# Kernel tuning notes

Measured on AMD Instinct MI355X. Metric: run time of the kernel, lower is better.

Reference implementation:

```python
import jax, jax.numpy as jnp
import numpy as np

B, S, D_IN, D, K, KU, L, M, H = 2, 1024, 64, 512, 16, 3, 2, 2, 2048
N_FFT = 2048  # next power of two >= 2*S - 1 (preconvolve padded_sl)
EPS = 1e-5


def setup_inputs() -> dict:
    key = jax.random.key(0)
    ks = jax.random.split(key, 8)
    # Hankel matrix Z[i,j] = 2 / ((i+j)^3 - (i+j)), i,j in 1..S; top-K eigh
    i = np.arange(1, S + 1, dtype=np.float64)
    s = i[:, None] + i[None, :]
    Z = 2.0 / (s ** 3 - s)
    evals, evecs = np.linalg.eigh(Z)
    sigma = jnp.asarray(evals[-K:], jnp.float32)          # (K,)
    phi = jnp.asarray(evecs[:, -K:], jnp.float32)         # (S, K)
    std = D ** -0.5
    return dict(
        inputs=jax.random.normal(ks[0], (B, S, D_IN), jnp.float32),
        sigma=sigma,
        phi=phi,
        in_proj_w=jax.random.normal(ks[1], (M, D, D_IN), jnp.float32) * (D_IN ** -0.5),
        rn_w=jnp.ones((M, L, D), jnp.float32),
        M_u=jax.random.uniform(ks[2], (M, L, KU, D, D), jnp.float32, -std, std),
        M_phi_plus=jax.random.normal(ks[3], (M, L, K, D, D), jnp.float32) * std,
        M_phi_minus=jax.random.normal(ks[4], (M, L, K, D, D), jnp.float32) * std,
        fc1_w=jax.random.normal(ks[5], (M, L, 2 * H, D), jnp.float32) * std,
        fc2_w=jax.random.normal(ks[6], (M, L, D, H), jnp.float32) * (H ** -0.5),
        out_proj_w=jax.random.normal(ks[7], (M, D_IN, D), jnp.float32) * std,
    )


def rmsnorm(x, w):
    return x * jax.lax.rsqrt(jnp.mean(x * x, axis=-1, keepdims=True) + EPS) * w


def compute_spectral(x, sigma, phi, mp, mm):
    # x: (B,S,D); phi: (S,K); mp/mm: (K,D,D)
    sgn = jnp.where(jnp.arange(S) % 2 == 0, 1.0, -1.0).astype(x.dtype)
    u2 = jnp.stack([x, x * sgn[None, :, None]], axis=-1)            # (B,S,D,2)
    U = jnp.fft.rfft(u2, n=N_FFT, axis=1)                           # (B,nf,D,2)
    Vf = jnp.fft.rfft(phi, n=N_FFT, axis=0)                         # (nf,K)
    Uc = jnp.fft.irfft(Vf[None, :, :, None, None] * U[:, :, None, :, :], n=N_FFT, axis=1)[:, :S]  # (B,S,K,D,2)
    Up = Uc[..., 0]
    Um = Uc[..., 1] * sgn[None, :, None, None]
    sig4 = sigma ** 0.25
    return (jnp.einsum('bskd,k,kdo->bso', Up, sig4, mp)
            + jnp.einsum('bskd,k,kdo->bso', Um, sig4, mm))


def compute_ar_u(mu, x):
    # y_t = sum_i x_{t-i} @ M_u[i]; mu: (KU,D,D)
    out = jnp.einsum('bsd,do->bso', x, mu[0])
    for i in range(1, KU):
        xi = jnp.pad(x[:, :S - i], ((0, 0), (i, 0), (0, 0)))
        out = out + jnp.einsum('bsd,do->bso', xi, mu[i])
    return out


def gated_mlp(x, w1, w2):
    y = x @ w1.T
    y, gate = jnp.split(y, 2, axis=-1)
    return (y * jax.nn.silu(gate)) @ w2.T


def reference(inputs, sigma, phi, in_proj_w, rn_w, M_u, M_phi_plus, M_phi_minus, fc1_w, fc2_w, out_proj_w):
    preds = jnp.zeros((B, S, D_IN), inputs.dtype)
    for m in range(M):  # ResidualSTU: sum of per-model predictions
        x = inputs @ in_proj_w[m].T
        for l in range(L):
            z = x
            h = rmsnorm(x, rn_w[m, l])
            spec = compute_spectral(h, sigma, phi, M_phi_plus[m, l], M_phi_minus[m, l])
            y_t = spec + compute_ar_u(M_u[m, l], h)  # use_ar_u=True, use_ar_y=False
            x = x + y_t
            x = x + gated_mlp(x, fc1_w[m, l], fc2_w[m, l])
            x = x + z
        preds = preds + x @ out_proj_w[m].T
    return preds
```

## Files before the change

kernel.cpp:

```cpp
#include <hip/hip_runtime.h>
#include <hip/hip_bf16.h>

typedef _Float16 f16;
typedef _Float16 half8 __attribute__((ext_vector_type(8)));
typedef float f32x4 __attribute__((ext_vector_type(4)));

#define S_LEN 1024
#define DMODEL 512
#define NFFT   2048
#define RPB    2048
#define RTOT   4096
#define CPS    1064
#define NROW   2048
#define NPART  4

__device__ __forceinline__ float2 mkf2(float a, float b) { float2 r; r.x = a; r.y = b; return r; }
__device__ __forceinline__ int zp(int i) { return i + (i >> 5); }

__device__ __forceinline__ void gl16(const f16* g, f16* l) {
  __builtin_amdgcn_global_load_lds((const __attribute__((address_space(1))) void*)g,
                                   (__attribute__((address_space(3))) void*)l, 16, 0, 0);
}

template<bool INV>
__device__ __forceinline__ void fft2048(float2* z, const float2* __restrict__ tw, int tid) {
  for (int i = tid; i < 2048; i += 256) {
    int j = (int)(__brev((unsigned)i) >> 21);
    if (i < j) { float2 a = z[zp(i)]; z[zp(i)] = z[zp(j)]; z[zp(j)] = a; }
  }
  __syncthreads();
#pragma unroll
  for (int sl = 1; sl <= 9; sl += 2) {
    const int h = 1 << (sl - 1);
    for (int q = tid; q < 512; q += 256) {
      int j = q & (h - 1);
      int base = (q >> (sl - 1)) << (sl + 1);
      int i0 = base + j;
      float2 a0 = z[zp(i0)], a1 = z[zp(i0 + h)], a2 = z[zp(i0 + 2 * h)], a3 = z[zp(i0 + 3 * h)];
      float2 w1 = tw[j << (11 - sl)];
      float2 w2 = tw[j << (10 - sl)];
      float2 w3 = tw[(j + h) << (10 - sl)];
      if (INV) { w1.y = -w1.y; w2.y = -w2.y; w3.y = -w3.y; }
      float tr, ti;
      tr = a1.x * w1.x - a1.y * w1.y; ti = a1.x * w1.y + a1.y * w1.x;
      float2 b0 = mkf2(a0.x + tr, a0.y + ti), b1 = mkf2(a0.x - tr, a0.y - ti);
      tr = a3.x * w1.x - a3.y * w1.y; ti = a3.x * w1.y + a3.y * w1.x;
      float2 b2 = mkf2(a2.x + tr, a2.y + ti), b3 = mkf2(a2.x - tr, a2.y - ti);
      tr = b2.x * w2.x - b2.y * w2.y; ti = b2.x * w2.y + b2.y * w2.x;
      z[zp(i0)]         = mkf2(b0.x + tr, b0.y + ti);
      z[zp(i0 + 2 * h)] = mkf2(b0.x - tr, b0.y - ti);
      tr = b3.x * w3.x - b3.y * w3.y; ti = b3.x * w3.y + b3.y * w3.x;
      z[zp(i0 + h)]     = mkf2(b1.x + tr, b1.y + ti);
      z[zp(i0 + 3 * h)] = mkf2(b1.x - tr, b1.y - ti);
    }
    __syncthreads();
  }
  for (int j = tid; j < 1024; j += 256) {
    float2 w = tw[j];
    if (INV) w.y = -w.y;
    float2 a = z[zp(j)], b = z[zp(j + 1024)];
    float tr = b.x * w.x - b.y * w.y, ti = b.x * w.y + b.y * w.x;
    z[zp(j)]        = mkf2(a.x + tr, a.y + ti);
    z[zp(j + 1024)] = mkf2(a.x - tr, a.y - ti);
  }
  __syncthreads();
}

__global__ void k_twiddle(float2* tw) {
  int i = blockIdx.x * 256 + threadIdx.x;
  if (i < 1024) {
    float ang = -6.2831853071795864769f * (float)i / 2048.0f;
    tw[i] = mkf2(cosf(ang), sinf(ang));
  }
}

__global__ void k_fft_phi(const float* __restrict__ phi, float2* __restrict__ Vf,
                          const float2* __restrict__ tw) {
  __shared__ float2 z[2112];
  int tid = threadIdx.x;
  int k0 = blockIdx.x * 2;
  for (int t = tid; t < 1024; t += 256)
    z[zp(t)] = *(const float2*)(phi + (size_t)t * 16 + k0);
  for (int t = 1024 + tid; t < 2048; t += 256) z[zp(t)] = mkf2(0.f, 0.f);
  __syncthreads();
  fft2048<false>(z, tw, tid);
  for (int f = tid; f <= 1024; f += 256) {
    float2 zf = z[zp(f)], zc = z[zp((2048 - f) & 2047)];
    Vf[(size_t)k0 * 1025 + f]       = mkf2(0.5f * (zf.x + zc.x), 0.5f * (zf.y - zc.y));
    Vf[(size_t)(k0 + 1) * 1025 + f] = mkf2(0.5f * (zf.y + zc.y), 0.5f * (zc.x - zf.x));
  }
}

__global__ void k_cpcm(const float2* __restrict__ Vf, const float* __restrict__ sigma,
                       float2* __restrict__ cpcm) {
  int idx = blockIdx.x * 256 + threadIdx.x;
  if (idx >= 32 * CPS) return;
  int kb = idx / CPS, f = idx - kb * CPS;
  int k = kb & 15;
  float s = powf(sigma[k], 0.25f) * (1.0f / 2048.0f);
  float2 v = mkf2(0.f, 0.f);
  if (f == 0) {
    float dc = Vf[(size_t)k * 1025].x;
    float ny = Vf[(size_t)k * 1025 + 1024].x;
    v = (kb < 16) ? mkf2(s * dc, s * ny) : mkf2(s * ny, s * dc);
  } else if (f <= 1023) {
    if (kb < 16) {
      v = Vf[(size_t)k * 1025 + f];
    } else {
      float2 t = Vf[(size_t)k * 1025 + (1024 - f)];
      v = mkf2(t.x, -t.y);
    }
    v.x *= s; v.y *= s;
  }
  cpcm[idx] = v;
}

__global__ void k_cast(const float* __restrict__ mp, const float* __restrict__ mm,
                       const float* __restrict__ mu, const float* __restrict__ fc1,
                       const float* __restrict__ fc2,
                       f16* __restrict__ Wsp, f16* __restrict__ Wu,
                       f16* __restrict__ Wf1, f16* __restrict__ Wf2) {
  __shared__ float T[64][65];
  int blk = blockIdx.x, tid = threadIdx.x;
  if (blk < 2048) {
    int mat = blk >> 6, tile = blk & 63;
    int d0 = (tile >> 3) * 64, o0 = (tile & 7) * 64;
    const float* src = (mat < 16) ? (mp + (size_t)mat * 262144)
                                  : (mm + (size_t)(mat - 16) * 262144);
    for (int q = tid; q < 4096; q += 256) {
      int i = q >> 6, j = q & 63;
      T[i][j] = src[(size_t)(d0 + i) * 512 + o0 + j];
    }
    __syncthreads();
    for (int q = tid; q < 4096; q += 256) {
      int i = q >> 6, j = q & 63;
      Wsp[(size_t)(mat * 512 + o0 + i) * 512 + d0 + j] = (f16)T[j][i];
    }
  } else if (blk < 2240) {
    int q0 = blk - 2048;
    int ip = q0 >> 6, tile = q0 & 63;
    int d0 = (tile >> 3) * 64, o0 = (tile & 7) * 64;
    const float* src = mu + (size_t)(2 - ip) * 262144;
    for (int q = tid; q < 4096; q += 256) {
      int i = q >> 6, j = q & 63;
      T[i][j] = src[(size_t)(d0 + i) * 512 + o0 + j];
    }
    __syncthreads();
    for (int q = tid; q < 4096; q += 256) {
      int i = q >> 6, j = q & 63;
      Wu[(size_t)(o0 + i) * 1536 + ip * 512 + d0 + j] = (f16)T[j][i];
    }
  } else if (blk < 3264) {
    int q0 = blk - 2240;
    size_t e = ((size_t)q0 * 256 + tid) * 8;
    int jj = (int)(e >> 9), col = (int)(e & 511);
    int srow = (jj & 1) ? (2048 + (jj >> 1)) : (jj >> 1);
    const float4* s = (const float4*)(fc1 + (size_t)srow * 512 + col);
    float4 a = s[0], b = s[1];
    union { f16 h[8]; uint4 u; } pk;
    pk.h[0] = (f16)a.x; pk.h[1] = (f16)a.y; pk.h[2] = (f16)a.z; pk.h[3] = (f16)a.w;
    pk.h[4] = (f16)b.x; pk.h[5] = (f16)b.y; pk.h[6] = (f16)b.z; pk.h[7] = (f16)b.w;
    *(uint4*)(Wf1 + (size_t)jj * 512 + col) = pk.u;
  } else {
    int q0 = blk - 3264;
    size_t e = ((size_t)q0 * 256 + tid) * 8;
    const float4* s = (const float4*)(fc2 + e);
    float4 a = s[0], b = s[1];
    union { f16 h[8]; uint4 u; } pk;
    pk.h[0] = (f16)a.x; pk.h[1] = (f16)a.y; pk.h[2] = (f16)a.z; pk.h[3] = (f16)a.w;
    pk.h[4] = (f16)b.x; pk.h[5] = (f16)b.y; pk.h[6] = (f16)b.z; pk.h[7] = (f16)b.w;
    *(uint4*)(Wf2 + e) = pk.u;
  }
}

__global__ void k_rmsnorm(const f16* __restrict__ x, const float* __restrict__ w,
                          f16* __restrict__ hb2) {
  int tid = threadIdx.x, l = tid & 63, wv = tid >> 6;
  int r = blockIdx.x * 4 + wv;
  int b = r >> 10, t = r & 1023;
  const f16* xr = x + (size_t)r * 512;
  f16* hr = hb2 + (size_t)(b * 1026 + 2 + t) * 512;
  float v[8]; float ss = 0.f;
#pragma unroll
  for (int j = 0; j < 8; ++j) { v[j] = (float)xr[j * 64 + l]; ss += v[j] * v[j]; }
#pragma unroll
  for (int o = 32; o; o >>= 1) ss += __shfl_xor(ss, o, 64);
  float rn = rsqrtf(ss * (1.f / 512.f) + 1e-5f);
#pragma unroll
  for (int j = 0; j < 8; ++j) {
    float hv = v[j] * rn * w[j * 64 + l];
    hr[j * 64 + l] = (f16)hv;
  }
}

__global__ void k_fft_fwd(const f16* __restrict__ hb2, f16* __restrict__ Xbf,
                          const float2* __restrict__ tw) {
  __shared__ float2 z[2112];
  int tid = threadIdx.x;
  int b = blockIdx.x >> 8;
  int d0 = (blockIdx.x & 255) * 2;
  for (int t = tid; t < 1024; t += 256) {
    union { unsigned v; f16 q[2]; } w;
    w.v = *(const unsigned*)(hb2 + (size_t)(b * 1026 + 2 + t) * 512 + d0);
    z[zp(t)] = mkf2((float)w.q[0], (float)w.q[1]);
  }
  for (int t = 1024 + tid; t < 2048; t += 256) z[zp(t)] = mkf2(0.f, 0.f);
  __syncthreads();
  fft2048<false>(z, tw, tid);
  for (int f = tid; f <= 1024; f += 256) {
    float2 zf = z[zp(f)], zc = z[zp((2048 - f) & 2047)];
    float x0r = 0.5f * (zf.x + zc.x), x0i = 0.5f * (zf.y - zc.y);
    float x1r = 0.5f * (zf.y + zc.y), x1i = 0.5f * (zc.x - zf.x);
    union { f16 h2[2]; unsigned u; } pr, pi;
    pr.h2[0] = (f16)x0r; pr.h2[1] = (f16)x1r;
    pi.h2[0] = (f16)x0i; pi.h2[1] = (f16)x1i;
    if (f == 0) {
      *(unsigned*)(Xbf + (size_t)(b * RPB) * 512 + d0) = pr.u;
    } else if (f == 1024) {
      *(unsigned*)(Xbf + (size_t)(b * RPB + 1) * 512 + d0) = pr.u;
    } else {
      *(unsigned*)(Xbf + (size_t)(b * RPB + 2 * f) * 512 + d0)     = pr.u;
      *(unsigned*)(Xbf + (size_t)(b * RPB + 2 * f + 1) * 512 + d0) = pi.u;
    }
  }
}

__global__ void k_fft_inv(const f16* __restrict__ P, f16* __restrict__ spec,
                          const float2* __restrict__ tw) {
  __shared__ float2 z[2112];
  int tid = threadIdx.x;
  int b = blockIdx.x >> 8;
  int o0 = (blockIdx.x & 255) * 2;
  for (int fp = tid; fp < 512; fp += 256) {
    int f0 = fp * 2;
    size_t base0 = (size_t)o0 * RTOT + (size_t)b * RPB + 2 * f0;
    float s0r[2] = {0.f, 0.f}, s0i[2] = {0.f, 0.f};
    float s1r[2] = {0.f, 0.f}, s1i[2] = {0.f, 0.f};
#pragma unroll
    for (int g = 0; g < NPART; ++g) {
      const f16* Pg = P + (size_t)g * 512 * RTOT;
      union { uint2 u; f16 h[4]; } ua, uc;
      ua.u = *(const uint2*)(Pg + base0);
      uc.u = *(const uint2*)(Pg + base0 + RTOT);
      s0r[0] += (float)ua.h[0]; s0i[0] += (float)ua.h[1];
      s0r[1] += (float)ua.h[2]; s0i[1] += (float)ua.h[3];
      s1r[0] += (float)uc.h[0]; s1i[0] += (float)uc.h[1];
      s1r[1] += (float)uc.h[2]; s1i[1] += (float)uc.h[3];
    }
    if (fp == 0) {
      z[zp(0)]    = mkf2(s0r[0], s1r[0]);
      z[zp(1024)] = mkf2(s0i[0], s1i[0]);
    } else {
      z[zp(f0)]        = mkf2(s0r[0] - s1i[0], s0i[0] + s1r[0]);
      z[zp(2048 - f0)] = mkf2(s0r[0] + s1i[0], s1r[0] - s0i[0]);
    }
    int f1 = f0 + 1;
    z[zp(f1)]        = mkf2(s0r[1] - s1i[1], s0i[1] + s1r[1]);
    z[zp(2048 - f1)] = mkf2(s0r[1] + s1i[1], s1r[1] - s0i[1]);
  }
  __syncthreads();
  fft2048<true>(z, tw, tid);
  for (int t = tid; t < 1024; t += 256) {
    float2 v = z[zp(t)];
    union { f16 h[2]; unsigned u; } pk;
    pk.h[0] = (f16)v.x; pk.h[1] = (f16)v.y;
    *(unsigned*)(spec + (size_t)(b * 1024 + t) * 512 + o0) = pk.u;
  }
}

template<int MODE, int MR, int NR>
__device__ __forceinline__ void stage(const f16* __restrict__ A, const f16* __restrict__ B0,
                                      int r0, int c0, int bz, int tid, int s,
                                      f16* As, f16* Bs) {
  constexpr int LDA = (MODE == 0) ? 512 : (MODE == 1) ? 1536 : (MODE == 2) ? 512 : 2048;
  const int kA = (MODE == 0) ? ((s & 7) * 64) : s * 64;
  const int rowl = tid >> 3;
  const int lc8 = ((tid & 7) ^ (rowl & 7)) * 8;
  f16* lA = As + ((tid >> 6) << 9);
  f16* lB = Bs + ((tid >> 6) << 9);
#pragma unroll
  for (int i = 0; i < MR; ++i) {
    int row = i * 32 + rowl;
    gl16(A + (size_t)(r0 + row) * LDA + kA + lc8, lA + i * 2048);
  }
#pragma unroll
  for (int i = 0; i < NR; ++i) {
    int row = i * 32 + rowl;
    const f16* bs;
    if constexpr (MODE == 0) {
      int kb = bz * 8 + (s >> 3);
      bs = B0 + (size_t)(kb * 512 + c0 + row) * 512 + (s & 7) * 64 + lc8;
    } else if constexpr (MODE == 1) {
      int ip = s >> 3, d0 = (s & 7) * 64;
      int rr = c0 + row;
      int b = rr >> 10, t = rr & 1023;
      bs = B0 + (size_t)(b * 1026 + t + ip) * 512 + d0 + lc8;
    } else {
      constexpr int LDB = (MODE == 2) ? 512 : 2048;
      bs = B0 + (size_t)(c0 + row) * LDB + s * 64 + lc8;
    }
    gl16(bs, lB + i * 2048);
  }
}

template<int MR, int NR>
__device__ __forceinline__ void mma_step(const f16* As, const f16* Bs, int l, int wr, int wc,
                                         f32x4 acc[MR][NR]) {
  const int lr = l & 15, kg = l >> 4, sw = l & 7;
#pragma unroll
  for (int kk = 0; kk < 2; ++kk) {
    half8 af[MR], bf[NR];
    const int pc8 = (((kk * 4 + kg) ^ sw) << 3);
#pragma unroll
    for (int m = 0; m < MR; ++m)
      af[m] = *(const half8*)(As + (wr * (MR * 16) + m * 16 + lr) * 64 + pc8);
#pragma unroll
    for (int n = 0; n < NR; ++n)
      bf[n] = *(const half8*)(Bs + (wc * (NR * 16) + n * 16 + lr) * 64 + pc8);
#pragma unroll
    for (int m = 0; m < MR; ++m)
#pragma unroll
      for (int n = 0; n < NR; ++n)
        acc[m][n] = __builtin_amdgcn_mfma_f32_16x16x32_f16(af[m], bf[n], acc[m][n], 0, 0, 0);
  }
}

template<int MODE, int MR, int NR>
__global__ __launch_bounds__(256, (MODE == 0) ? 2 : ((MODE == 2) ? 3 : 4))
void k_gemm(const f16* __restrict__ A, const f16* __restrict__ B0,
            const float* __restrict__ aux0, const f16* auxA, const f16* auxB,
            f16* __restrict__ outH) {
  __shared__ __align__(16) f16 As[MR * 32 * 64];
  __shared__ __align__(16) f16 Bs[NR * 32 * 64];
  const int tid = threadIdx.x, l = tid & 63, wvi = tid >> 6;
  const int wr = wvi >> 1, wc = wvi & 1;
  int bx, by, bz;
  if constexpr (MODE == 0) {
    int wg = (int)blockIdx.x;
    wg = (wg & 7) * 64 + (wg >> 3);
    bz = wg >> 7; int rem = wg & 127;
    by = rem >> 2; bx = rem & 3;
  } else { bx = blockIdx.x; by = blockIdx.y; bz = 0; }
  const int r0 = by * (MR * 32), c0 = bx * (NR * 32);
  constexpr int KS = (MODE == 0) ? 64 : (MODE == 1) ? 24 : (MODE == 2) ? 8 : 32;

  f32x4 acc[MR][NR];
  f32x4 crun[MR][NR];
  f32x4 zz = {0.f, 0.f, 0.f, 0.f};
#pragma unroll
  for (int m = 0; m < MR; ++m)
#pragma unroll
    for (int n = 0; n < NR; ++n) { acc[m][n] = zz; crun[m][n] = zz; }

  for (int s = 0; s < KS; ++s) {
    __syncthreads();
    stage<MODE, MR, NR>(A, B0, r0, c0, bz, tid, s, As, Bs);
    __syncthreads();
    mma_step<MR, NR>(As, Bs, l, wr, wc, acc);
    if constexpr (MODE == 0) {
      if ((s & 7) == 7) {
        int kb = bz * 8 + (s >> 3);
#pragma unroll
        for (int m = 0; m < MR; ++m) {
          int R = r0 + wr * (MR * 16) + m * 16 + ((l >> 4) << 2);
          int rb = R & (RPB - 1);
          bool dc = (rb == 0);
          float4 cs = *(const float4*)(aux0 + (size_t)kb * (CPS * 2) + (rb >> 1) * 2);
          float t1 = dc ? 0.f : cs.y;
          float t2 = dc ? cs.y : cs.x;
#pragma unroll
          for (int n = 0; n < NR; ++n) {
            f32x4 p = acc[m][n];
            crun[m][n].x += cs.x * p.x - t1 * p.y;
            crun[m][n].y += t2 * p.y + t1 * p.x;
            crun[m][n].z += cs.z * p.z - cs.w * p.w;
            crun[m][n].w += cs.z * p.w + cs.w * p.z;
            acc[m][n] = zz;
          }
        }
      }
    }
  }

  if constexpr (MODE == 0) {
    f16* P = outH + (size_t)bz * (512ull * RTOT);
#pragma unroll
    for (int m = 0; m < MR; ++m) {
      int R0 = r0 + wr * (MR * 16) + m * 16 + ((l >> 4) << 2);
#pragma unroll
      for (int n = 0; n < NR; ++n) {
        int o = c0 + wc * (NR * 16) + n * 16 + (l & 15);
        union { f16 h[4]; uint2 u; } pk;
        pk.h[0] = (f16)crun[m][n].x; pk.h[1] = (f16)crun[m][n].y;
        pk.h[2] = (f16)crun[m][n].z; pk.h[3] = (f16)crun[m][n].w;
        *(uint2*)(P + (size_t)o * RTOT + R0) = pk.u;
      }
    }
  } else if constexpr (MODE == 1) {
#pragma unroll
    for (int m = 0; m < MR; ++m) {
      int o0 = r0 + wr * (MR * 16) + m * 16 + ((l >> 4) << 2);
#pragma unroll
      for (int n = 0; n < NR; ++n) {
        int r = c0 + wc * (NR * 16) + n * 16 + (l & 15);
        union { uint2 u; f16 h[4]; } xv, sv;
        xv.u = *(const uint2*)(auxA + (size_t)r * 512 + o0);
        sv.u = *(const uint2*)(auxB + (size_t)r * 512 + o0);
        f32x4 a = acc[m][n];
        union { f16 h[4]; uint2 u; } pk;
        pk.h[0] = (f16)((float)xv.h[0] + (float)sv.h[0] + a.x);
        pk.h[1] = (f16)((float)xv.h[1] + (float)sv.h[1] + a.y);
        pk.h[2] = (f16)((float)xv.h[2] + (float)sv.h[2] + a.z);
        pk.h[3] = (f16)((float)xv.h[3] + (float)sv.h[3] + a.w);
        *(uint2*)(outH + (size_t)r * 512 + o0) = pk.u;
      }
    }
  } else if constexpr (MODE == 2) {
#pragma unroll
    for (int m = 0; m < MR; ++m) {
      int jj0 = r0 + wr * (MR * 16) + m * 16 + ((l >> 4) << 2);
      int h2 = jj0 >> 1;
#pragma unroll
      for (int n = 0; n < NR; ++n) {
        int r = c0 + wc * (NR * 16) + n * 16 + (l & 15);
        f32x4 a = acc[m][n];
        float v0 = a.x * (a.y / (1.f + __expf(-a.y)));
        float v1 = a.z * (a.w / (1.f + __expf(-a.w)));
        union { f16 h[2]; unsigned u; } pk;
        pk.h[0] = (f16)v0; pk.h[1] = (f16)v1;
        *(unsigned*)(outH + (size_t)r * 2048 + h2) = pk.u;
      }
    }
  } else {
#pragma unroll
    for (int m = 0; m < MR; ++m) {
      int o0 = r0 + wr * (MR * 16) + m * 16 + ((l >> 4) << 2);
#pragma unroll
      for (int n = 0; n < NR; ++n) {
        int r = c0 + wc * (NR * 16) + n * 16 + (l & 15);
        union { uint2 u; f16 h[4]; } xv, x1v;
        xv.u  = *(const uint2*)(auxA + (size_t)r * 512 + o0);
        x1v.u = *(const uint2*)(auxB + (size_t)r * 512 + o0);
        f32x4 a = acc[m][n];
        union { f16 h[4]; uint2 u; } pk;
        pk.h[0] = (f16)((float)xv.h[0] + (float)x1v.h[0] + a.x);
        pk.h[1] = (f16)((float)xv.h[1] + (float)x1v.h[1] + a.y);
        pk.h[2] = (f16)((float)xv.h[2] + (float)x1v.h[2] + a.z);
        pk.h[3] = (f16)((float)xv.h[3] + (float)x1v.h[3] + a.w);
        *(uint2*)(outH + (size_t)r * 512 + o0) = pk.u;
      }
    }
  }
}

__global__ void k_inproj(const float* __restrict__ inp, const float* __restrict__ W,
                         f16* __restrict__ x) {
  __shared__ float row[64];
  int r = blockIdx.x, tid = threadIdx.x;
  if (tid < 64) row[tid] = inp[(size_t)r * 64 + tid];
  __syncthreads();
  for (int o = tid; o < 512; o += 256) {
    const float* wr = W + (size_t)o * 64;
    float acc = 0.f;
#pragma unroll 8
    for (int q = 0; q < 64; ++q) acc += row[q] * wr[q];
    x[(size_t)r * 512 + o] = (f16)acc;
  }
}

__global__ void k_outproj(const f16* __restrict__ x, const float* __restrict__ W,
                          float* out, int add) {
  __shared__ float row[512];
  int r = blockIdx.x, tid = threadIdx.x;
  for (int i = tid; i < 512; i += 256) row[i] = (float)x[(size_t)r * 512 + i];
  __syncthreads();
  int o = tid >> 2, part = tid & 3;
  const float* wr = W + (size_t)o * 512 + part * 128;
  const float* rp = row + part * 128;
  float acc = 0.f;
#pragma unroll 16
  for (int q = 0; q < 128; ++q) acc += rp[q] * wr[q];
  acc += __shfl_xor(acc, 1, 64);
  acc += __shfl_xor(acc, 2, 64);
  if (part == 0) {
    if (add) out[(size_t)r * 64 + o] += acc;
    else     out[(size_t)r * 64 + o] = acc;
  }
}

extern "C" void kernel_launch(void* const* d_in, const int* in_sizes, int n_in,
                              void* d_out, int out_size, void* d_ws, size_t ws_size,
                              hipStream_t stream) {
  const float* inputs    = (const float*)d_in[0];
  const float* sigma     = (const float*)d_in[1];
  const float* phi       = (const float*)d_in[2];
  const float* in_proj_w = (const float*)d_in[3];
  const float* rn_w      = (const float*)d_in[4];
  const float* M_u       = (const float*)d_in[5];
  const float* M_phi_p   = (const float*)d_in[6];
  const float* M_phi_m   = (const float*)d_in[7];
  const float* fc1       = (const float*)d_in[8];
  const float* fc2       = (const float*)d_in[9];
  const float* out_proj_w= (const float*)d_in[10];
  float* out = (float*)d_out;

  char* ws = (char*)d_ws;
  size_t off = 0;
  auto alloc = [&](size_t bytes) -> void* {
    void* p = ws + off;
    off += (bytes + 255) & ~(size_t)255;
    return p;
  };
  float2* tw   = (float2*)alloc(1024 * 8);
  float2* Vf   = (float2*)alloc((size_t)16 * 1025 * 8);
  float2* cpcm = (float2*)alloc((size_t)32 * CPS * 8);
  f16*    x    = (f16*)alloc((size_t)NROW * 512 * 2);
  f16*    hb2  = (f16*)alloc((size_t)2052 * 512 * 2);
  f16*    x1   = (f16*)alloc((size_t)NROW * 512 * 2);
  f16*    spec = (f16*)alloc((size_t)NROW * 512 * 2);
  f16*    Xbf  = (f16*)alloc((size_t)RTOT * 512 * 2);
  f16*    P    = (f16*)alloc((size_t)NPART * 512 * RTOT * 2);
  f16*    g1   = (f16*)alloc((size_t)NROW * 2048 * 2);
  f16*    Wsp  = (f16*)alloc((size_t)16384 * 512 * 2);
  f16*    Wu   = (f16*)alloc((size_t)512 * 1536 * 2);
  f16*    Wf1  = (f16*)alloc((size_t)4096 * 512 * 2);
  f16*    Wf2  = (f16*)alloc((size_t)512 * 2048 * 2);
  if (off > ws_size) return;

  hipMemsetAsync(hb2, 0, 2 * 512 * sizeof(f16), stream);
  hipMemsetAsync(hb2 + (size_t)1026 * 512, 0, 2 * 512 * sizeof(f16), stream);
  k_twiddle<<<4, 256, 0, stream>>>(tw);
  k_fft_phi<<<8, 256, 0, stream>>>(phi, Vf, tw);
  k_cpcm<<<133, 256, 0, stream>>>(Vf, sigma, cpcm);

  for (int m = 0; m < 2; ++m) {
    k_inproj<<<NROW, 256, 0, stream>>>(inputs, in_proj_w + (size_t)m * 512 * 64, x);
    for (int li = 0; li < 2; ++li) {
      int ml = m * 2 + li;
      k_cast<<<3776, 256, 0, stream>>>(
          M_phi_p + (size_t)ml * 16 * 262144, M_phi_m + (size_t)ml * 16 * 262144,
          M_u + (size_t)ml * 3 * 262144, fc1 + (size_t)ml * 4096 * 512,
          fc2 + (size_t)ml * 512 * 2048, Wsp, Wu, Wf1, Wf2);
      k_rmsnorm<<<512, 256, 0, stream>>>(x, rn_w + (size_t)ml * 512, hb2);
      k_fft_fwd<<<512, 256, 0, stream>>>(hb2, Xbf, tw);
      k_gemm<0, 4, 4><<<dim3(512), 256, 0, stream>>>(Xbf, Wsp, (const float*)cpcm,
                                                     nullptr, nullptr, P);
      k_fft_inv<<<512, 256, 0, stream>>>(P, spec, tw);
      k_gemm<1, 2, 2><<<dim3(32, 8), 256, 0, stream>>>(Wu, hb2, nullptr, x, spec, x1);
      k_gemm<2, 4, 4><<<dim3(16, 32), 256, 0, stream>>>(Wf1, x1, nullptr,
                                                        nullptr, nullptr, g1);
      k_gemm<3, 2, 2><<<dim3(32, 8), 256, 0, stream>>>(Wf2, g1, nullptr, x, x1, x);
    }
    k_outproj<<<NROW, 256, 0, stream>>>(x, out_proj_w + (size_t)m * 64 * 512, out, m);
  }
}
```

Before: 853.2 us.

## Use radix-8 FFT stages and fuse forward FFT with weight cast kernel

The 2048-point FFT now runs three radix-8 passes plus a final radix-4 pass instead of five radix-4 passes plus a radix-2 pass, which cuts the number of barriers and shared-memory round trips. The forward FFT is also merged into the weight-cast kernel as extra workgroups, with rmsnorm moved ahead of it. This lets the FFT work overlap with the memory-bound cast and removes one launch. The radix-8 butterflies need more registers per thread, and the merged kernel's shared-memory size is set by the larger of its two branches.

```diff
diff --git a/kernel.cpp b/kernel.cpp
--- a/kernel.cpp
+++ b/kernel.cpp
@@ -16,6 +16,11 @@
 
 __device__ __forceinline__ float2 mkf2(float a, float b) { float2 r; r.x = a; r.y = b; return r; }
 __device__ __forceinline__ int zp(int i) { return i + (i >> 5); }
+__device__ __forceinline__ float2 cmul(float2 w, float2 b) {
+  return mkf2(b.x * w.x - b.y * w.y, b.x * w.y + b.y * w.x);
+}
+__device__ __forceinline__ float2 f2a(float2 a, float2 b) { return mkf2(a.x + b.x, a.y + b.y); }
+__device__ __forceinline__ float2 f2s(float2 a, float2 b) { return mkf2(a.x - b.x, a.y - b.y); }
 
 __device__ __forceinline__ void gl16(const f16* g, f16* l) {
   __builtin_amdgcn_global_load_lds((const __attribute__((address_space(1))) void*)g,
@@ -30,38 +35,53 @@
   }
   __syncthreads();
 #pragma unroll
-  for (int sl = 1; sl <= 9; sl += 2) {
+  for (int r8 = 0; r8 < 3; ++r8) {
+    const int sl = 1 + 3 * r8;
     const int h = 1 << (sl - 1);
-    for (int q = tid; q < 512; q += 256) {
+    {
+      int q = tid;
       int j = q & (h - 1);
-      int base = (q >> (sl - 1)) << (sl + 1);
-      int i0 = base + j;
-      float2 a0 = z[zp(i0)], a1 = z[zp(i0 + h)], a2 = z[zp(i0 + 2 * h)], a3 = z[zp(i0 + 3 * h)];
-      float2 w1 = tw[j << (11 - sl)];
-      float2 w2 = tw[j << (10 - sl)];
-      float2 w3 = tw[(j + h) << (10 - sl)];
-      if (INV) { w1.y = -w1.y; w2.y = -w2.y; w3.y = -w3.y; }
-      float tr, ti;
-      tr = a1.x * w1.x - a1.y * w1.y; ti = a1.x * w1.y + a1.y * w1.x;
-      float2 b0 = mkf2(a0.x + tr, a0.y + ti), b1 = mkf2(a0.x - tr, a0.y - ti);
-      tr = a3.x * w1.x - a3.y * w1.y; ti = a3.x * w1.y + a3.y * w1.x;
-      float2 b2 = mkf2(a2.x + tr, a2.y + ti), b3 = mkf2(a2.x - tr, a2.y - ti);
-      tr = b2.x * w2.x - b2.y * w2.y; ti = b2.x * w2.y + b2.y * w2.x;
-      z[zp(i0)]         = mkf2(b0.x + tr, b0.y + ti);
-      z[zp(i0 + 2 * h)] = mkf2(b0.x - tr, b0.y - ti);
-      tr = b3.x * w3.x - b3.y * w3.y; ti = b3.x * w3.y + b3.y * w3.x;
-      z[zp(i0 + h)]     = mkf2(b1.x + tr, b1.y + ti);
-      z[zp(i0 + 3 * h)] = mkf2(b1.x - tr, b1.y - ti);
+      int i0 = ((q >> (sl - 1)) << (sl + 2)) + j;
+      float2 a0 = z[zp(i0)],         a1 = z[zp(i0 + h)];
+      float2 a2 = z[zp(i0 + 2 * h)], a3 = z[zp(i0 + 3 * h)];
+      float2 a4 = z[zp(i0 + 4 * h)], a5 = z[zp(i0 + 5 * h)];
+      float2 a6 = z[zp(i0 + 6 * h)], a7 = z[zp(i0 + 7 * h)];
+      float2 wA  = tw[j << (11 - sl)];
+      float2 wB0 = tw[j << (10 - sl)];
+      float2 wB1 = tw[(j + h) << (10 - sl)];
+      float2 wC0 = tw[j << (9 - sl)];
+      float2 wC1 = tw[(j + h) << (9 - sl)];
+      float2 wC2 = tw[(j + 2 * h) << (9 - sl)];
+      float2 wC3 = tw[(j + 3 * h) << (9 - sl)];
+      if (INV) {
+        wA.y = -wA.y; wB0.y = -wB0.y; wB1.y = -wB1.y;
+        wC0.y = -wC0.y; wC1.y = -wC1.y; wC2.y = -wC2.y; wC3.y = -wC3.y;
+      }
+      float2 t;
+      t = cmul(wA, a1); float2 b0 = f2a(a0, t), b1 = f2s(a0, t);
+      t = cmul(wA, a3); float2 b2 = f2a(a2, t), b3 = f2s(a2, t);
+      t = cmul(wA, a5); float2 b4 = f2a(a4, t), b5 = f2s(a4, t);
+      t = cmul(wA, a7); float2 b6 = f2a(a6, t), b7 = f2s(a6, t);
+      t = cmul(wB0, b2); float2 c0 = f2a(b0, t), c2 = f2s(b0, t);
+      t = cmul(wB1, b3); float2 c1 = f2a(b1, t), c3 = f2s(b1, t);
+      t = cmul(wB0, b6); float2 c4 = f2a(b4, t), c6 = f2s(b4, t);
+      t = cmul(wB1, b7); float2 c5 = f2a(b5, t), c7 = f2s(b5, t);
+      t = cmul(wC0, c4); z[zp(i0)]         = f2a(c0, t); z[zp(i0 + 4 * h)] = f2s(c0, t);
+      t = cmul(wC1, c5); z[zp(i0 + h)]     = f2a(c1, t); z[zp(i0 + 5 * h)] = f2s(c1, t);
+      t = cmul(wC2, c6); z[zp(i0 + 2 * h)] = f2a(c2, t); z[zp(i0 + 6 * h)] = f2s(c2, t);
+      t = cmul(wC3, c7); z[zp(i0 + 3 * h)] = f2a(c3, t); z[zp(i0 + 7 * h)] = f2s(c3, t);
     }
     __syncthreads();
   }
-  for (int j = tid; j < 1024; j += 256) {
-    float2 w = tw[j];
-    if (INV) w.y = -w.y;
-    float2 a = z[zp(j)], b = z[zp(j + 1024)];
-    float tr = b.x * w.x - b.y * w.y, ti = b.x * w.y + b.y * w.x;
-    z[zp(j)]        = mkf2(a.x + tr, a.y + ti);
-    z[zp(j + 1024)] = mkf2(a.x - tr, a.y - ti);
+  for (int q = tid; q < 512; q += 256) {
+    float2 a0 = z[zp(q)], a1 = z[zp(q + 512)], a2 = z[zp(q + 1024)], a3 = z[zp(q + 1536)];
+    float2 w1 = tw[q << 1], w2 = tw[q], w3 = tw[q + 512];
+    if (INV) { w1.y = -w1.y; w2.y = -w2.y; w3.y = -w3.y; }
+    float2 t;
+    t = cmul(w1, a1); float2 b0 = f2a(a0, t), b1 = f2s(a0, t);
+    t = cmul(w1, a3); float2 b2 = f2a(a2, t), b3 = f2s(a2, t);
+    t = cmul(w2, b2); z[zp(q)]        = f2a(b0, t); z[zp(q + 1024)] = f2s(b0, t);
+    t = cmul(w3, b3); z[zp(q + 512)]  = f2a(b1, t); z[zp(q + 1536)] = f2s(b1, t);
   }
   __syncthreads();
 }
@@ -115,13 +135,48 @@
   cpcm[idx] = v;
 }
 
-__global__ void k_cast(const float* __restrict__ mp, const float* __restrict__ mm,
-                       const float* __restrict__ mu, const float* __restrict__ fc1,
-                       const float* __restrict__ fc2,
-                       f16* __restrict__ Wsp, f16* __restrict__ Wu,
-                       f16* __restrict__ Wf1, f16* __restrict__ Wf2) {
-  __shared__ float T[64][65];
-  int blk = blockIdx.x, tid = threadIdx.x;
+__global__ __launch_bounds__(256)
+void k_fwdcast(const f16* __restrict__ hb2, f16* __restrict__ Xbf,
+               const float2* __restrict__ tw,
+               const float* __restrict__ mp, const float* __restrict__ mm,
+               const float* __restrict__ mu, const float* __restrict__ fc1,
+               const float* __restrict__ fc2,
+               f16* __restrict__ Wsp, f16* __restrict__ Wu,
+               f16* __restrict__ Wf1, f16* __restrict__ Wf2) {
+  __shared__ __align__(16) char smem[16896];
+  int wg = (int)blockIdx.x, tid = threadIdx.x;
+  if (wg < 512) {
+    float2* z = (float2*)smem;
+    int b = wg >> 8;
+    int d0 = (wg & 255) * 2;
+    for (int t = tid; t < 1024; t += 256) {
+      union { unsigned v; f16 q[2]; } w;
+      w.v = *(const unsigned*)(hb2 + (size_t)(b * 1026 + 2 + t) * 512 + d0);
+      z[zp(t)] = mkf2((float)w.q[0], (float)w.q[1]);
+    }
+    for (int t = 1024 + tid; t < 2048; t += 256) z[zp(t)] = mkf2(0.f, 0.f);
+    __syncthreads();
+    fft2048<false>(z, tw, tid);
+    for (int f = tid; f <= 1024; f += 256) {
+      float2 zf = z[zp(f)], zc = z[zp((2048 - f) & 2047)];
+      float x0r = 0.5f * (zf.x + zc.x), x0i = 0.5f * (zf.y - zc.y);
+      float x1r = 0.5f * (zf.y + zc.y), x1i = 0.5f * (zc.x - zf.x);
+      union { f16 h2[2]; unsigned u; } pr, pi;
+      pr.h2[0] = (f16)x0r; pr.h2[1] = (f16)x1r;
+      pi.h2[0] = (f16)x0i; pi.h2[1] = (f16)x1i;
+      if (f == 0) {
+        *(unsigned*)(Xbf + (size_t)(b * RPB) * 512 + d0) = pr.u;
+      } else if (f == 1024) {
+        *(unsigned*)(Xbf + (size_t)(b * RPB + 1) * 512 + d0) = pr.u;
+      } else {
+        *(unsigned*)(Xbf + (size_t)(b * RPB + 2 * f) * 512 + d0)     = pr.u;
+        *(unsigned*)(Xbf + (size_t)(b * RPB + 2 * f + 1) * 512 + d0) = pi.u;
+      }
+    }
+    return;
+  }
+  float* T = (float*)smem;
+  int blk = wg - 512;
   if (blk < 2048) {
     int mat = blk >> 6, tile = blk & 63;
     int d0 = (tile >> 3) * 64, o0 = (tile & 7) * 64;
@@ -129,12 +184,12 @@
                                   : (mm + (size_t)(mat - 16) * 262144);
     for (int q = tid; q < 4096; q += 256) {
       int i = q >> 6, j = q & 63;
-      T[i][j] = src[(size_t)(d0 + i) * 512 + o0 + j];
+      T[i * 65 + j] = src[(size_t)(d0 + i) * 512 + o0 + j];
     }
     __syncthreads();
     for (int q = tid; q < 4096; q += 256) {
       int i = q >> 6, j = q & 63;
-      Wsp[(size_t)(mat * 512 + o0 + i) * 512 + d0 + j] = (f16)T[j][i];
+      Wsp[(size_t)(mat * 512 + o0 + i) * 512 + d0 + j] = (f16)T[j * 65 + i];
     }
   } else if (blk < 2240) {
     int q0 = blk - 2048;
@@ -143,12 +198,12 @@
     const float* src = mu + (size_t)(2 - ip) * 262144;
     for (int q = tid; q < 4096; q += 256) {
       int i = q >> 6, j = q & 63;
-      T[i][j] = src[(size_t)(d0 + i) * 512 + o0 + j];
+      T[i * 65 + j] = src[(size_t)(d0 + i) * 512 + o0 + j];
     }
     __syncthreads();
     for (int q = tid; q < 4096; q += 256) {
       int i = q >> 6, j = q & 63;
-      Wu[(size_t)(o0 + i) * 1536 + ip * 512 + d0 + j] = (f16)T[j][i];
+      Wu[(size_t)(o0 + i) * 1536 + ip * 512 + d0 + j] = (f16)T[j * 65 + i];
     }
   } else if (blk < 3264) {
     int q0 = blk - 2240;
@@ -190,38 +245,6 @@
   for (int j = 0; j < 8; ++j) {
     float hv = v[j] * rn * w[j * 64 + l];
     hr[j * 64 + l] = (f16)hv;
-  }
-}
-
-__global__ void k_fft_fwd(const f16* __restrict__ hb2, f16* __restrict__ Xbf,
-                          const float2* __restrict__ tw) {
-  __shared__ float2 z[2112];
-  int tid = threadIdx.x;
-  int b = blockIdx.x >> 8;
-  int d0 = (blockIdx.x & 255) * 2;
-  for (int t = tid; t < 1024; t += 256) {
-    union { unsigned v; f16 q[2]; } w;
-    w.v = *(const unsigned*)(hb2 + (size_t)(b * 1026 + 2 + t) * 512 + d0);
-    z[zp(t)] = mkf2((float)w.q[0], (float)w.q[1]);
-  }
-  for (int t = 1024 + tid; t < 2048; t += 256) z[zp(t)] = mkf2(0.f, 0.f);
-  __syncthreads();
-  fft2048<false>(z, tw, tid);
-  for (int f = tid; f <= 1024; f += 256) {
-    float2 zf = z[zp(f)], zc = z[zp((2048 - f) & 2047)];
-    float x0r = 0.5f * (zf.x + zc.x), x0i = 0.5f * (zf.y - zc.y);
-    float x1r = 0.5f * (zf.y + zc.y), x1i = 0.5f * (zc.x - zf.x);
-    union { f16 h2[2]; unsigned u; } pr, pi;
-    pr.h2[0] = (f16)x0r; pr.h2[1] = (f16)x1r;
-    pi.h2[0] = (f16)x0i; pi.h2[1] = (f16)x1i;
-    if (f == 0) {
-      *(unsigned*)(Xbf + (size_t)(b * RPB) * 512 + d0) = pr.u;
-    } else if (f == 1024) {
-      *(unsigned*)(Xbf + (size_t)(b * RPB + 1) * 512 + d0) = pr.u;
-    } else {
-      *(unsigned*)(Xbf + (size_t)(b * RPB + 2 * f) * 512 + d0)     = pr.u;
-      *(unsigned*)(Xbf + (size_t)(b * RPB + 2 * f + 1) * 512 + d0) = pi.u;
-    }
   }
 }
 
@@ -537,12 +560,12 @@
     k_inproj<<<NROW, 256, 0, stream>>>(inputs, in_proj_w + (size_t)m * 512 * 64, x);
     for (int li = 0; li < 2; ++li) {
       int ml = m * 2 + li;
-      k_cast<<<3776, 256, 0, stream>>>(
+      k_rmsnorm<<<512, 256, 0, stream>>>(x, rn_w + (size_t)ml * 512, hb2);
+      k_fwdcast<<<512 + 3776, 256, 0, stream>>>(
+          hb2, Xbf, tw,
           M_phi_p + (size_t)ml * 16 * 262144, M_phi_m + (size_t)ml * 16 * 262144,
           M_u + (size_t)ml * 3 * 262144, fc1 + (size_t)ml * 4096 * 512,
           fc2 + (size_t)ml * 512 * 2048, Wsp, Wu, Wf1, Wf2);
-      k_rmsnorm<<<512, 256, 0, stream>>>(x, rn_w + (size_t)ml * 512, hb2);
-      k_fft_fwd<<<512, 256, 0, stream>>>(hb2, Xbf, tw);
       k_gemm<0, 4, 4><<<dim3(512), 256, 0, stream>>>(Xbf, Wsp, (const float*)cpcm,
                                                      nullptr, nullptr, P);
       k_fft_inv<<<512, 256, 0, stream>>>(P, spec, tw);
```

After: 827.6 us. 3.0% less time.
